# Optimization experiments

Measured on AMD Instinct MI355X. Metric: run time of the kernel, lower is better.

Reference implementation:

```python
import jax, jax.numpy as jnp
import numpy as np

N = 50000        # nodes
DEG = 5          # avg directed degree before symmetrization
F_IN = 512       # node features
HID = 64         # hardcoded hidden width in H2GCN
C = 32           # num_classes
E1_MAX = 800000  # padded 1-hop edge count
E2_MAX = 6000000 # padded 2-hop edge count


def _pad(a, L, dtype):
    out = np.zeros(L, dtype=dtype)
    n = min(len(a), L)
    out[:n] = a[:n]
    return out


def _build_graph(seed=0):
    """Build symmetric 1-hop adjacency A1 (no self loops) and strict 2-hop A2,
    both symmetrically normalized D^-1/2 A D^-1/2, as padded COO edge lists."""
    rng = np.random.default_rng(seed)
    src = rng.integers(0, N, N * DEG)
    dst = rng.integers(0, N, N * DEG)
    row = np.concatenate([src, dst])  # symmetrize
    col = np.concatenate([dst, src])
    m = row != col                    # drop self loops (A - I > 0)
    row, col = row[m], col[m]
    key = np.unique(row.astype(np.int64) * N + col)  # dedupe, sorted by row
    row = (key // N).astype(np.int64)
    col = (key % N).astype(np.int64)
    deg = np.bincount(row, minlength=N)  # symmetric -> row sums == col sums
    dinv = np.where(deg > 0, deg.astype(np.float64) ** -0.5, 0.0).astype(np.float32)
    val1 = dinv[row] * dinv[col]
    # --- compose A@A via CSR expansion (edges sorted by row) ---
    rowptr = np.concatenate([[0], np.cumsum(deg)])
    lens = deg[col]                     # out-degree of each edge's endpoint
    total = int(lens.sum())
    starts = rowptr[col]
    grp = np.repeat(np.cumsum(lens) - lens, lens)
    idx = np.repeat(starts, lens) + (np.arange(total) - grp)
    u2 = np.repeat(row, lens)
    w2 = col[idx]
    key2 = np.unique(u2.astype(np.int64) * N + w2)
    r2 = key2 // N
    c2 = key2 % N
    # strict 2-hop: remove self loops and 1-hop edges
    keep = (r2 != c2) & (~np.isin(key2, key, assume_unique=True))
    r2, c2 = r2[keep], c2[keep]
    deg2 = np.bincount(r2, minlength=N)
    d2inv = np.where(deg2 > 0, deg2.astype(np.float64) ** -0.5, 0.0).astype(np.float32)
    val2 = d2inv[r2] * d2inv[c2]
    return (
        _pad(row, E1_MAX, np.int32), _pad(col, E1_MAX, np.int32), _pad(val1, E1_MAX, np.float32),
        _pad(r2, E2_MAX, np.int32), _pad(c2, E2_MAX, np.int32), _pad(val2, E2_MAX, np.float32),
    )


def setup_inputs() -> dict:
    key = jax.random.key(0)
    k = jax.random.split(key, 6)
    e1r, e1c, e1v, e2r, e2c, e2v = _build_graph(0)
    return {
        "x": jax.random.normal(k[0], (N, F_IN), dtype=jnp.float32),
        "e1_row": jnp.asarray(e1r), "e1_col": jnp.asarray(e1c), "e1_val": jnp.asarray(e1v),
        "e2_row": jnp.asarray(e2r), "e2_col": jnp.asarray(e2c), "e2_val": jnp.asarray(e2v),
        "W1": jax.random.normal(k[1], (F_IN, HID), dtype=jnp.float32) * (1.0 / np.sqrt(F_IN)),
        "b1": jax.random.normal(k[2], (HID,), dtype=jnp.float32) * 0.01,
        "W2": jax.random.normal(k[3], (3 * HID, C), dtype=jnp.float32) * (1.0 / np.sqrt(3 * HID)),
        "b2": jax.random.normal(k[4], (C,), dtype=jnp.float32) * 0.01,
    }


def _spmm(row, col, val, R):
    # sparse [N,N] @ dense [N,H]: gather source rows, scale, scatter-add to dest
    return jax.ops.segment_sum(val[:, None] * R[col], row, num_segments=N)


def reference(x, e1_row, e1_col, e1_val, e2_row, e2_col, e2_val, W1, b1, W2, b2):
    R = jax.nn.relu(x @ W1 + b1)            # [N, 64]
    Rs = [R]
    for _ in range(2):                       # two rounds of hop aggregation
        R1 = _spmm(e1_row, e1_col, e1_val, R)
        R2 = _spmm(e2_row, e2_col, e2_val, R)
        R = jnp.maximum(R1, R2)              # max-pool combine
        Rs.append(R)
    R_final = jnp.concatenate(Rs, axis=1)    # [N, 192]
    # dropout is identity in eval mode
    return jax.nn.log_softmax(R_final @ W2 + b2, axis=1)
```

## Files before the change

### kernel.cpp

```cpp
#include <hip/hip_runtime.h>

#define NN 50000
#define FIN 512
#define HID 64
#define NC 32

typedef __attribute__((ext_vector_type(8))) short short8;
typedef __attribute__((ext_vector_type(4))) float f32x4;

__device__ __forceinline__ unsigned short bf16rne(float f) {
  unsigned u = __float_as_uint(f);
  u = u + 0x7FFFu + ((u >> 16) & 1u);
  return (unsigned short)(u >> 16);
}
__device__ __forceinline__ float bf2f(unsigned short s) {
  return __uint_as_float(((unsigned)s) << 16);
}
__device__ __forceinline__ unsigned cvt_pk_bf16(float lo, float hi) {
  unsigned d;
  asm("v_cvt_pk_bf16_f32 %0, %1, %2" : "=v"(d) : "v"(lo), "v"(hi));
  return d;
}

__global__ void w1_pack_kernel(const float* __restrict__ W1,
                               unsigned short* __restrict__ W1p) {
  const int t = blockIdx.x * blockDim.x + threadIdx.x;
  if (t >= 16 * 4 * 64) return;
  const int lane = t & 63, nb = (t >> 6) & 3, ks = t >> 8;
  const int col = nb * 16 + (lane & 15);
  const int k0 = ks * 32 + (lane >> 4) * 8;
  float f[8];
#pragma unroll
  for (int j = 0; j < 8; ++j) f[j] = W1[(size_t)(k0 + j) * HID + col];
  uint4 d;
  d.x = cvt_pk_bf16(f[0], f[1]);
  d.y = cvt_pk_bf16(f[2], f[3]);
  d.z = cvt_pk_bf16(f[4], f[5]);
  d.w = cvt_pk_bf16(f[6], f[7]);
  *(uint4*)(W1p + (size_t)t * 8) = d;
}

__global__ __launch_bounds__(256) void gemm1_relu_kernel(
    const float* __restrict__ x, const unsigned short* __restrict__ W1p,
    const float* __restrict__ b1, float* __restrict__ R0,
    unsigned short* __restrict__ R0b) {
  const int t = threadIdx.x;
  const int w = t >> 6, lane = t & 63;
  const int arow = blockIdx.x * 64 + w * 16 + (lane & 15);
  const size_t rowoff = (arow < NN) ? (size_t)arow * FIN : 0;
  const float* xp = x + rowoff + (lane >> 4) * 8;
  f32x4 acc0 = {0.f, 0.f, 0.f, 0.f}, acc1 = acc0, acc2 = acc0, acc3 = acc0;
#pragma unroll
  for (int ks = 0; ks < 16; ++ks) {
    const float4 xa = *(const float4*)(xp);
    const float4 xb = *(const float4*)(xp + 4);
    xp += 32;
    uint4 ad;
    ad.x = cvt_pk_bf16(xa.x, xa.y);
    ad.y = cvt_pk_bf16(xa.z, xa.w);
    ad.z = cvt_pk_bf16(xb.x, xb.y);
    ad.w = cvt_pk_bf16(xb.z, xb.w);
    const short8 af = __builtin_bit_cast(short8, ad);
    const short8 b0 = *(const short8*)(W1p + ((size_t)(ks * 4 + 0) * 64 + lane) * 8);
    const short8 b1f = *(const short8*)(W1p + ((size_t)(ks * 4 + 1) * 64 + lane) * 8);
    const short8 b2 = *(const short8*)(W1p + ((size_t)(ks * 4 + 2) * 64 + lane) * 8);
    const short8 b3 = *(const short8*)(W1p + ((size_t)(ks * 4 + 3) * 64 + lane) * 8);
    acc0 = __builtin_amdgcn_mfma_f32_16x16x32_bf16(af, b0, acc0, 0, 0, 0);
    acc1 = __builtin_amdgcn_mfma_f32_16x16x32_bf16(af, b1f, acc1, 0, 0, 0);
    acc2 = __builtin_amdgcn_mfma_f32_16x16x32_bf16(af, b2, acc2, 0, 0, 0);
    acc3 = __builtin_amdgcn_mfma_f32_16x16x32_bf16(af, b3, acc3, 0, 0, 0);
  }
  const int orow = blockIdx.x * 64 + w * 16 + (lane >> 4) * 4;
  const int ocol = lane & 15;
#define EPI(NB, ACC)                                                        \
  {                                                                         \
    const float bias = b1[NB * 16 + ocol];                                  \
    _Pragma("unroll") for (int i = 0; i < 4; ++i) {                         \
      const int r = orow + i;                                               \
      if (r < NN) {                                                         \
        const float v = fmaxf(ACC[i] + bias, 0.f);                          \
        R0[(size_t)r * HID + NB * 16 + ocol] = v;                           \
        R0b[(size_t)r * HID + NB * 16 + ocol] = bf16rne(v);                 \
      }                                                                     \
    }                                                                       \
  }
  EPI(0, acc0) EPI(1, acc1) EPI(2, acc2) EPI(3, acc3)
#undef EPI
}

__global__ void build_rowptr_kernel(const int* __restrict__ row,
                                    const float* __restrict__ val,
                                    const int E, int* __restrict__ ptr) {
  const int e = blockIdx.x * blockDim.x + threadIdx.x;
  if (e >= E) return;
  const int c = (val[e] != 0.f) ? row[e] : NN;
  const int p = (e == 0) ? -1 : ((val[e - 1] != 0.f) ? row[e - 1] : NN);
  for (int r = p + 1; r <= c; ++r) ptr[r] = e;
  if (e == E - 1) {
    for (int r = c + 1; r <= NN; ++r) ptr[r] = E;
  }
}

template <int BLK>
__device__ __forceinline__ float2 seg_pair(const int* __restrict__ col,
                                           const float* __restrict__ val,
                                           int s, int t,
                                           const char* __restrict__ Rbc,
                                           uint2* __restrict__ meta,
                                           const int lane, const unsigned laneoff) {
  float a0 = 0.f, a1 = 0.f;
  const int half = lane >> 5;
  for (int e = s; e < t; e += BLK) {
    const int idx = e + lane;
    if (lane < BLK) {
      unsigned cw = 0u, vw = 0u;
      if (idx < t) { cw = (unsigned)col[idx]; vw = __float_as_uint(val[idx]); }
      meta[lane] = make_uint2(cw, vw);
    }
#pragma unroll
    for (int i = 0; i < BLK / 2; ++i) {
      const uint2 m = meta[2 * i + half];
      const float v = __uint_as_float(m.y);
      const unsigned off = m.x * 128u + laneoff;
      const unsigned gw = *(const unsigned*)(Rbc + off);
      a0 = fmaf(v, __uint_as_float(gw << 16), a0);
      a1 = fmaf(v, __uint_as_float(gw & 0xffff0000u), a1);
    }
  }
  return make_float2(a0, a1);
}

template <int OUTMODE>
__global__ __launch_bounds__(256) void agg_kernel(
    const int* __restrict__ c1, const float* __restrict__ v1, const int* __restrict__ p1,
    const int* __restrict__ c2, const float* __restrict__ v2, const int* __restrict__ p2,
    const unsigned short* __restrict__ Rb,
    float* __restrict__ outf, unsigned short* __restrict__ outb) {
  __shared__ uint2 meta[4][64];
  const int wslot = threadIdx.x >> 6;
  const int wid = (int)((blockIdx.x * blockDim.x + threadIdx.x) >> 6);
  if (wid >= NN) return;
  const int lane = threadIdx.x & 63;
  const unsigned laneoff = (unsigned)(lane & 31) << 2;
  const char* Rbc = (const char*)Rb;
  const float2 h1 = seg_pair<16>(c1, v1, p1[wid], p1[wid + 1], Rbc, meta[wslot], lane, laneoff);
  const float2 h2 = seg_pair<64>(c2, v2, p2[wid], p2[wid + 1], Rbc, meta[wslot], lane, laneoff);
  const float t1e = h1.x + __shfl_xor(h1.x, 32, 64);
  const float t1o = h1.y + __shfl_xor(h1.y, 32, 64);
  const float t2e = h2.x + __shfl_xor(h2.x, 32, 64);
  const float t2o = h2.y + __shfl_xor(h2.y, 32, 64);
  const int half = lane >> 5;
  const float r = half ? fmaxf(t1o, t2o) : fmaxf(t1e, t2e);
  const size_t oidx = (size_t)wid * HID + 2 * (lane & 31) + half;
  if (OUTMODE == 0) outb[oidx] = bf16rne(r);
  else              outf[oidx] = r;
}

__global__ void final_kernel(const float* __restrict__ R0,
                             const unsigned short* __restrict__ R1b,
                             const float* __restrict__ R2,
                             const float* __restrict__ W2,
                             const float* __restrict__ b2, float* __restrict__ out) {
  __shared__ float w2s[192 * 32];
  __shared__ float fs[8][192];
  const int t = threadIdx.x;
  const int node0 = blockIdx.x * 8;
  for (int i = t; i < 192 * 32; i += 256) w2s[i] = W2[i];
  for (int i = t; i < 8 * 192; i += 256) {
    const int n = i / 192, k = i % 192;
    const int node = node0 + n;
    float v = 0.f;
    if (node < NN) {
      v = (k < 64)  ? R0[(size_t)node * 64 + k]
        : (k < 128) ? bf2f(R1b[(size_t)node * 64 + (k - 64)])
                    : R2[(size_t)node * 64 + (k - 128)];
    }
    fs[n][k] = v;
  }
  __syncthreads();
  const int n = t >> 5, c = t & 31;
  const int node = node0 + n;
  float acc = b2[c];
#pragma unroll 8
  for (int k = 0; k < 192; ++k) acc += fs[n][k] * w2s[k * 32 + c];
  float m = acc;
  for (int off = 16; off; off >>= 1) m = fmaxf(m, __shfl_xor(m, off, 32));
  const float ex = __expf(acc - m);
  float ssum = ex;
  for (int off = 16; off; off >>= 1) ssum += __shfl_xor(ssum, off, 32);
  if (node < NN) out[(size_t)node * 32 + c] = (acc - m) - __logf(ssum);
}

extern "C" void kernel_launch(void* const* d_in, const int* in_sizes, int n_in,
                              void* d_out, int out_size, void* d_ws, size_t ws_size,
                              hipStream_t stream) {
  const float* x  = (const float*)d_in[0];
  const int*   e1r = (const int*)d_in[1];
  const int*   e1c = (const int*)d_in[2];
  const float* e1v = (const float*)d_in[3];
  const int*   e2r = (const int*)d_in[4];
  const int*   e2c = (const int*)d_in[5];
  const float* e2v = (const float*)d_in[6];
  const float* W1 = (const float*)d_in[7];
  const float* b1 = (const float*)d_in[8];
  const float* W2 = (const float*)d_in[9];
  const float* b2 = (const float*)d_in[10];
  float* out = (float*)d_out;
  const int E1 = in_sizes[1];
  const int E2 = in_sizes[4];

  char* wsb = (char*)d_ws;
  const size_t RSZ = (size_t)NN * HID;
  const size_t need = RSZ * 4 * 2 + RSZ * 2 * 2 + 2 * (NN + 1) * sizeof(int)
                    + (size_t)FIN * HID * 2;
  if (ws_size < need) return;
  float*          R0  = (float*)wsb;
  float*          R2  = (float*)(wsb + RSZ * 4);
  unsigned short* R0b = (unsigned short*)(wsb + RSZ * 8);
  unsigned short* R1b = (unsigned short*)(wsb + RSZ * 8 + RSZ * 2);
  int*            p1  = (int*)(wsb + RSZ * 8 + RSZ * 4);
  int*            p2  = p1 + (NN + 1);
  unsigned short* W1p = (unsigned short*)(p2 + (NN + 1));

  w1_pack_kernel<<<16, 256, 0, stream>>>(W1, W1p);

  gemm1_relu_kernel<<<(NN + 63) / 64, 256, 0, stream>>>(x, W1p, b1, R0, R0b);

  build_rowptr_kernel<<<(E1 + 255) / 256, 256, 0, stream>>>(e1r, e1v, E1, p1);
  build_rowptr_kernel<<<(E2 + 255) / 256, 256, 0, stream>>>(e2r, e2v, E2, p2);

  const int aggb = (NN * 64) / 256;
  agg_kernel<0><<<aggb, 256, 0, stream>>>(e1c, e1v, p1, e2c, e2v, p2, R0b, (float*)nullptr, R1b);
  agg_kernel<1><<<aggb, 256, 0, stream>>>(e1c, e1v, p1, e2c, e2v, p2, R1b, R2, (unsigned short*)nullptr);

  final_kernel<<<(NN + 7) / 8, 256, 0, stream>>>(R0, R1b, R2, W2, b2, out);
}
```

Before: 396.2 us.

## Rewrite final projection with bf16 MFMA and keep all hidden states in bf16

The final 192x32 projection plus log_softmax now runs on 16x16x32 bf16 MFMA instructions using a pre-packed W2 fragment layout, replacing the scalar LDS dot-product kernel. R0 and R2 are no longer written as fp32; all three hidden states are stored only in bf16, which removes the redundant fp32 writes and halves their read traffic. The cost is lower precision in the classifier inputs and weights, which could cause small accuracy drift.

```diff
diff --git a/kernel.cpp b/kernel.cpp
--- a/kernel.cpp
+++ b/kernel.cpp
@@ -13,37 +13,43 @@
   u = u + 0x7FFFu + ((u >> 16) & 1u);
   return (unsigned short)(u >> 16);
 }
-__device__ __forceinline__ float bf2f(unsigned short s) {
-  return __uint_as_float(((unsigned)s) << 16);
-}
 __device__ __forceinline__ unsigned cvt_pk_bf16(float lo, float hi) {
   unsigned d;
   asm("v_cvt_pk_bf16_f32 %0, %1, %2" : "=v"(d) : "v"(lo), "v"(hi));
   return d;
 }
 
-__global__ void w1_pack_kernel(const float* __restrict__ W1,
-                               unsigned short* __restrict__ W1p) {
+__global__ void pack_kernel(const float* __restrict__ W1, const float* __restrict__ W2,
+                            unsigned short* __restrict__ W1p,
+                            unsigned short* __restrict__ W2p) {
   const int t = blockIdx.x * blockDim.x + threadIdx.x;
-  if (t >= 16 * 4 * 64) return;
-  const int lane = t & 63, nb = (t >> 6) & 3, ks = t >> 8;
-  const int col = nb * 16 + (lane & 15);
-  const int k0 = ks * 32 + (lane >> 4) * 8;
-  float f[8];
-#pragma unroll
-  for (int j = 0; j < 8; ++j) f[j] = W1[(size_t)(k0 + j) * HID + col];
-  uint4 d;
-  d.x = cvt_pk_bf16(f[0], f[1]);
-  d.y = cvt_pk_bf16(f[2], f[3]);
-  d.z = cvt_pk_bf16(f[4], f[5]);
-  d.w = cvt_pk_bf16(f[6], f[7]);
-  *(uint4*)(W1p + (size_t)t * 8) = d;
+  if (t < 16 * 4 * 64) {
+    const int lane = t & 63, nb = (t >> 6) & 3, ks = t >> 8;
+    const int col = nb * 16 + (lane & 15);
+    const int k0 = ks * 32 + (lane >> 4) * 8;
+    uint4 d;
+    d.x = cvt_pk_bf16(W1[(size_t)(k0 + 0) * HID + col], W1[(size_t)(k0 + 1) * HID + col]);
+    d.y = cvt_pk_bf16(W1[(size_t)(k0 + 2) * HID + col], W1[(size_t)(k0 + 3) * HID + col]);
+    d.z = cvt_pk_bf16(W1[(size_t)(k0 + 4) * HID + col], W1[(size_t)(k0 + 5) * HID + col]);
+    d.w = cvt_pk_bf16(W1[(size_t)(k0 + 6) * HID + col], W1[(size_t)(k0 + 7) * HID + col]);
+    *(uint4*)(W1p + (size_t)t * 8) = d;
+  } else if (t < 4096 + 6 * 2 * 64) {
+    const int t2 = t - 4096;
+    const int lane = t2 & 63, nb = (t2 >> 6) & 1, ks = t2 >> 7;
+    const int col = nb * 16 + (lane & 15);
+    const int k0 = ks * 32 + (lane >> 4) * 8;
+    uint4 d;
+    d.x = cvt_pk_bf16(W2[(size_t)(k0 + 0) * NC + col], W2[(size_t)(k0 + 1) * NC + col]);
+    d.y = cvt_pk_bf16(W2[(size_t)(k0 + 2) * NC + col], W2[(size_t)(k0 + 3) * NC + col]);
+    d.z = cvt_pk_bf16(W2[(size_t)(k0 + 4) * NC + col], W2[(size_t)(k0 + 5) * NC + col]);
+    d.w = cvt_pk_bf16(W2[(size_t)(k0 + 6) * NC + col], W2[(size_t)(k0 + 7) * NC + col]);
+    *(uint4*)(W2p + (size_t)t2 * 8) = d;
+  }
 }
 
 __global__ __launch_bounds__(256) void gemm1_relu_kernel(
     const float* __restrict__ x, const unsigned short* __restrict__ W1p,
-    const float* __restrict__ b1, float* __restrict__ R0,
-    unsigned short* __restrict__ R0b) {
+    const float* __restrict__ b1, unsigned short* __restrict__ R0b) {
   const int t = threadIdx.x;
   const int w = t >> 6, lane = t & 63;
   const int arow = blockIdx.x * 64 + w * 16 + (lane & 15);
@@ -79,7 +85,6 @@
       const int r = orow + i;                                               \
       if (r < NN) {                                                         \
         const float v = fmaxf(ACC[i] + bias, 0.f);                          \
-        R0[(size_t)r * HID + NB * 16 + ocol] = v;                           \
         R0b[(size_t)r * HID + NB * 16 + ocol] = bf16rne(v);                 \
       }                                                                     \
     }                                                                       \
@@ -130,12 +135,10 @@
   return make_float2(a0, a1);
 }
 
-template <int OUTMODE>
 __global__ __launch_bounds__(256) void agg_kernel(
     const int* __restrict__ c1, const float* __restrict__ v1, const int* __restrict__ p1,
     const int* __restrict__ c2, const float* __restrict__ v2, const int* __restrict__ p2,
-    const unsigned short* __restrict__ Rb,
-    float* __restrict__ outf, unsigned short* __restrict__ outb) {
+    const unsigned short* __restrict__ Rb, unsigned short* __restrict__ outb) {
   __shared__ uint2 meta[4][64];
   const int wslot = threadIdx.x >> 6;
   const int wid = (int)((blockIdx.x * blockDim.x + threadIdx.x) >> 6);
@@ -151,44 +154,46 @@
   const float t2o = h2.y + __shfl_xor(h2.y, 32, 64);
   const int half = lane >> 5;
   const float r = half ? fmaxf(t1o, t2o) : fmaxf(t1e, t2e);
-  const size_t oidx = (size_t)wid * HID + 2 * (lane & 31) + half;
-  if (OUTMODE == 0) outb[oidx] = bf16rne(r);
-  else              outf[oidx] = r;
-}
-
-__global__ void final_kernel(const float* __restrict__ R0,
-                             const unsigned short* __restrict__ R1b,
-                             const float* __restrict__ R2,
-                             const float* __restrict__ W2,
-                             const float* __restrict__ b2, float* __restrict__ out) {
-  __shared__ float w2s[192 * 32];
-  __shared__ float fs[8][192];
+  outb[(size_t)wid * HID + 2 * (lane & 31) + half] = bf16rne(r);
+}
+
+__global__ __launch_bounds__(256) void final_kernel(
+    const unsigned short* __restrict__ R0b, const unsigned short* __restrict__ R1b,
+    const unsigned short* __restrict__ R2b, const unsigned short* __restrict__ W2p,
+    const float* __restrict__ b2, float* __restrict__ out) {
   const int t = threadIdx.x;
-  const int node0 = blockIdx.x * 8;
-  for (int i = t; i < 192 * 32; i += 256) w2s[i] = W2[i];
-  for (int i = t; i < 8 * 192; i += 256) {
-    const int n = i / 192, k = i % 192;
-    const int node = node0 + n;
-    float v = 0.f;
-    if (node < NN) {
-      v = (k < 64)  ? R0[(size_t)node * 64 + k]
-        : (k < 128) ? bf2f(R1b[(size_t)node * 64 + (k - 64)])
-                    : R2[(size_t)node * 64 + (k - 128)];
+  const int w = t >> 6, lane = t & 63;
+  const int node0 = blockIdx.x * 64 + w * 16;
+  const int arow = node0 + (lane & 15);
+  const size_t rbase = (size_t)(arow < NN ? arow : 0) * HID + (lane >> 4) * 8;
+  f32x4 acc0 = {0.f, 0.f, 0.f, 0.f}, acc1 = acc0;
+#define FSTEP(KS, SRC)                                                          \
+  {                                                                             \
+    const short8 af = *(const short8*)(SRC + rbase + (KS & 1) * 32);            \
+    const short8 bf0 = *(const short8*)(W2p + ((size_t)(KS * 2 + 0) * 64 + lane) * 8); \
+    const short8 bf1 = *(const short8*)(W2p + ((size_t)(KS * 2 + 1) * 64 + lane) * 8); \
+    acc0 = __builtin_amdgcn_mfma_f32_16x16x32_bf16(af, bf0, acc0, 0, 0, 0);     \
+    acc1 = __builtin_amdgcn_mfma_f32_16x16x32_bf16(af, bf1, acc1, 0, 0, 0);     \
+  }
+  FSTEP(0, R0b) FSTEP(1, R0b) FSTEP(2, R1b) FSTEP(3, R1b) FSTEP(4, R2b) FSTEP(5, R2b)
+#undef FSTEP
+  const float b2v0 = b2[lane & 15];
+  const float b2v1 = b2[16 + (lane & 15)];
+#pragma unroll
+  for (int i = 0; i < 4; ++i) {
+    const float l0 = acc0[i] + b2v0;
+    const float l1 = acc1[i] + b2v1;
+    float m = fmaxf(l0, l1);
+    for (int off = 1; off < 16; off <<= 1) m = fmaxf(m, __shfl_xor(m, off, 64));
+    float s = __expf(l0 - m) + __expf(l1 - m);
+    for (int off = 1; off < 16; off <<= 1) s += __shfl_xor(s, off, 64);
+    const float lse = m + __logf(s);
+    const int r = node0 + (lane >> 4) * 4 + i;
+    if (r < NN) {
+      out[(size_t)r * NC + (lane & 15)] = l0 - lse;
+      out[(size_t)r * NC + 16 + (lane & 15)] = l1 - lse;
     }
-    fs[n][k] = v;
-  }
-  __syncthreads();
-  const int n = t >> 5, c = t & 31;
-  const int node = node0 + n;
-  float acc = b2[c];
-#pragma unroll 8
-  for (int k = 0; k < 192; ++k) acc += fs[n][k] * w2s[k * 32 + c];
-  float m = acc;
-  for (int off = 16; off; off >>= 1) m = fmaxf(m, __shfl_xor(m, off, 32));
-  const float ex = __expf(acc - m);
-  float ssum = ex;
-  for (int off = 16; off; off >>= 1) ssum += __shfl_xor(ssum, off, 32);
-  if (node < NN) out[(size_t)node * 32 + c] = (acc - m) - __logf(ssum);
+  }
 }
 
 extern "C" void kernel_launch(void* const* d_in, const int* in_sizes, int n_in,
@@ -211,27 +216,27 @@
 
   char* wsb = (char*)d_ws;
   const size_t RSZ = (size_t)NN * HID;
-  const size_t need = RSZ * 4 * 2 + RSZ * 2 * 2 + 2 * (NN + 1) * sizeof(int)
-                    + (size_t)FIN * HID * 2;
+  const size_t need = RSZ * 2 * 3 + 2 * (NN + 1) * sizeof(int)
+                    + (size_t)4096 * 16 + (size_t)768 * 16;
   if (ws_size < need) return;
-  float*          R0  = (float*)wsb;
-  float*          R2  = (float*)(wsb + RSZ * 4);
-  unsigned short* R0b = (unsigned short*)(wsb + RSZ * 8);
-  unsigned short* R1b = (unsigned short*)(wsb + RSZ * 8 + RSZ * 2);
-  int*            p1  = (int*)(wsb + RSZ * 8 + RSZ * 4);
+  unsigned short* R0b = (unsigned short*)wsb;
+  unsigned short* R1b = (unsigned short*)(wsb + RSZ * 2);
+  unsigned short* R2b = (unsigned short*)(wsb + RSZ * 4);
+  int*            p1  = (int*)(wsb + RSZ * 6);
   int*            p2  = p1 + (NN + 1);
   unsigned short* W1p = (unsigned short*)(p2 + (NN + 1));
-
-  w1_pack_kernel<<<16, 256, 0, stream>>>(W1, W1p);
-
-  gemm1_relu_kernel<<<(NN + 63) / 64, 256, 0, stream>>>(x, W1p, b1, R0, R0b);
+  unsigned short* W2p = W1p + (size_t)4096 * 8;
+
+  pack_kernel<<<19, 256, 0, stream>>>(W1, W2, W1p, W2p);
+
+  gemm1_relu_kernel<<<(NN + 63) / 64, 256, 0, stream>>>(x, W1p, b1, R0b);
 
   build_rowptr_kernel<<<(E1 + 255) / 256, 256, 0, stream>>>(e1r, e1v, E1, p1);
   build_rowptr_kernel<<<(E2 + 255) / 256, 256, 0, stream>>>(e2r, e2v, E2, p2);
 
   const int aggb = (NN * 64) / 256;
-  agg_kernel<0><<<aggb, 256, 0, stream>>>(e1c, e1v, p1, e2c, e2v, p2, R0b, (float*)nullptr, R1b);
-  agg_kernel<1><<<aggb, 256, 0, stream>>>(e1c, e1v, p1, e2c, e2v, p2, R1b, R2, (unsigned short*)nullptr);
-
-  final_kernel<<<(NN + 7) / 8, 256, 0, stream>>>(R0, R1b, R2, W2, b2, out);
-}
+  agg_kernel<<<aggb, 256, 0, stream>>>(e1c, e1v, p1, e2c, e2v, p2, R0b, R1b);
+  agg_kernel<<<aggb, 256, 0, stream>>>(e1c, e1v, p1, e2c, e2v, p2, R1b, R2b);
+
+  final_kernel<<<(NN + 63) / 64, 256, 0, stream>>>(R0b, R1b, R2b, W2p, b2, out);
+}
```

Result: faster. 355.8 us (-10.2%).
